# Optimization experiments

Measured on AMD Instinct MI355X. Metric: run time of the kernel, lower is better.

Reference implementation:

```python
import jax, jax.numpy as jnp
import numpy as np

T, TRACE, CTX = 4096, 64, 64


def setup_inputs() -> dict:
    key = jax.random.key(0)
    k0, k1, k2, k3 = jax.random.split(key, 4)
    state_re = jax.random.normal(k0, (T, TRACE, CTX), dtype=jnp.float32)
    state_im = jax.random.normal(k1, (T, TRACE, CTX), dtype=jnp.float32)
    x_re = jax.random.normal(k2, (T, TRACE, CTX), dtype=jnp.float32)
    x_im = jax.random.normal(k3, (T, TRACE, CTX), dtype=jnp.float32)
    # deterministic FFA param init (init_deterministic)
    a = jnp.linspace(1e-6, 0.5, TRACE).astype(jnp.float32)
    b = (2.0 * jnp.pi / jnp.linspace(1.0, 1000.0, CTX)).astype(jnp.float32)
    i = jnp.ones((T,), dtype=jnp.int32)          # carry step counter
    j = jnp.arange(T, dtype=jnp.int32)           # incoming time offsets
    return {"state_re": state_re, "state_im": state_im, "x_re": x_re,
            "x_im": x_im, "a": a, "b": b, "i": i, "j": j}


def reference(state_re, state_im, x_re, x_im, a, b, i, j):
    # gamma(t) = exp((-|a| + i*b) * t) expanded in real arithmetic
    t = j.astype(jnp.float32)[:, None, None]              # [T,1,1]
    decay = jnp.exp(-jnp.abs(a)[None, :, None] * t)       # [T,TRACE,1]
    theta = b[None, None, :] * t                          # [T,1,CTX]
    g_re = decay * jnp.cos(theta)                         # [T,TRACE,CTX]
    g_im = decay * jnp.sin(theta)
    # state * gamma + x  (complex multiply-add)
    new_re = state_re * g_re - state_im * g_im + x_re
    new_im = state_re * g_im + state_im * g_re + x_im
    # output: complex state stacked as (..., 2) = (re, im), plus updated counter
    return jnp.stack([new_re, new_im], axis=-1), j + i
```

## Files before the change

### kernel.cpp

```cpp
#include <hip/hip_runtime.h>
#include <math.h>

#define T_DIM 4096
#define TRACE 64
#define CTX 64

__global__ __launch_bounds__(256) void ffm_kernel(
    const float* __restrict__ state_re,
    const float* __restrict__ state_im,
    const float* __restrict__ x_re,
    const float* __restrict__ x_im,
    const float* __restrict__ a,
    const float* __restrict__ b,
    const int*   __restrict__ ivec,
    const int*   __restrict__ jvec,
    float* __restrict__ out,
    float* __restrict__ out_cnt)
{
    const int t   = blockIdx.x;
    const int tid = threadIdx.x;
    const float tf = (float)jvec[t];

    __shared__ float s_cos[CTX];
    __shared__ float s_sin[CTX];
    __shared__ float s_dec[TRACE];

    if (tid < CTX) {
        float theta = b[tid] * tf;
        float s, c;
        sincosf(theta, &s, &c);
        s_cos[tid] = c;
        s_sin[tid] = s;
    } else if (tid < CTX + TRACE) {
        int tr = tid - CTX;
        s_dec[tr] = expf(-fabsf(a[tr]) * tf);
    }
    if (tid == 0) {
        out_cnt[t] = (float)(jvec[t] + ivec[t]);
    }
    __syncthreads();

    const size_t base = (size_t)t * (TRACE * CTX);
    const float4* sre = (const float4*)(state_re + base);
    const float4* sim = (const float4*)(state_im + base);
    const float4* xre = (const float4*)(x_re + base);
    const float4* xim = (const float4*)(x_im + base);
    float4* o = (float4*)(out + base * 2);

    #pragma unroll
    for (int k = 0; k < 4; ++k) {
        const int g  = tid + k * 256;
        const int e  = g * 4;
        const int tr = e >> 6;
        const int c0 = e & 63;

        const float dec = s_dec[tr];
        const float4 vre = sre[g];
        const float4 vim = sim[g];
        const float4 vxr = xre[g];
        const float4 vxi = xim[g];

        const float gr0 = dec * s_cos[c0 + 0], gi0 = dec * s_sin[c0 + 0];
        const float gr1 = dec * s_cos[c0 + 1], gi1 = dec * s_sin[c0 + 1];
        const float gr2 = dec * s_cos[c0 + 2], gi2 = dec * s_sin[c0 + 2];
        const float gr3 = dec * s_cos[c0 + 3], gi3 = dec * s_sin[c0 + 3];

        float4 o0, o1;
        o0.x = fmaf(vre.x, gr0, fmaf(-vim.x, gi0, vxr.x));
        o0.y = fmaf(vre.x, gi0, fmaf( vim.x, gr0, vxi.x));
        o0.z = fmaf(vre.y, gr1, fmaf(-vim.y, gi1, vxr.y));
        o0.w = fmaf(vre.y, gi1, fmaf( vim.y, gr1, vxi.y));
        o1.x = fmaf(vre.z, gr2, fmaf(-vim.z, gi2, vxr.z));
        o1.y = fmaf(vre.z, gi2, fmaf( vim.z, gr2, vxi.z));
        o1.z = fmaf(vre.w, gr3, fmaf(-vim.w, gi3, vxr.w));
        o1.w = fmaf(vre.w, gi3, fmaf( vim.w, gr3, vxi.w));

        o[2 * g + 0] = o0;
        o[2 * g + 1] = o1;
    }
}

extern "C" void kernel_launch(void* const* d_in, const int* in_sizes, int n_in,
                              void* d_out, int out_size, void* d_ws, size_t ws_size,
                              hipStream_t stream) {
    const float* state_re = (const float*)d_in[0];
    const float* state_im = (const float*)d_in[1];
    const float* x_re     = (const float*)d_in[2];
    const float* x_im     = (const float*)d_in[3];
    const float* a        = (const float*)d_in[4];
    const float* b        = (const float*)d_in[5];
    const int*   iv       = (const int*)d_in[6];
    const int*   jv       = (const int*)d_in[7];

    float* out     = (float*)d_out;
    float* out_cnt = out + (size_t)T_DIM * TRACE * CTX * 2;

    ffm_kernel<<<T_DIM, 256, 0, stream>>>(state_re, state_im, x_re, x_im,
                                          a, b, iv, jv, out, out_cnt);
}
```

Measured before the change: 326.5 us.

## Precompute gamma tables in a separate kernel and stream main pass with grid-stride nontemporal stores

Moves the per-timestep sincos/exp computation into a small prepass kernel that writes cos, sin and decay tables to workspace. The main kernel then becomes a persistent grid-stride loop over 2048 blocks that reads the tables from global memory and writes the output with nontemporal stores. The aim is to remove per-block shared-memory setup and the __syncthreads barrier, and to keep streamed output from polluting the cache. In exchange it adds a second kernel launch and extra table traffic, and it falls back to the old kernel when the workspace is too small.

```diff
diff --git a/kernel.cpp b/kernel.cpp
--- a/kernel.cpp
+++ b/kernel.cpp
@@ -3,19 +3,89 @@
 
 #define T_DIM 4096
 #define TRACE 64
-#define CTX 64
+#define CTX   64
+#define NELEM  (T_DIM * TRACE * CTX)
+#define NGROUP (NELEM / 4)
 
-__global__ __launch_bounds__(256) void ffm_kernel(
-    const float* __restrict__ state_re,
-    const float* __restrict__ state_im,
-    const float* __restrict__ x_re,
-    const float* __restrict__ x_im,
-    const float* __restrict__ a,
-    const float* __restrict__ b,
-    const int*   __restrict__ ivec,
-    const int*   __restrict__ jvec,
-    float* __restrict__ out,
-    float* __restrict__ out_cnt)
+typedef float f32x4 __attribute__((ext_vector_type(4)));
+
+__global__ __launch_bounds__(256) void ffm_tables(
+    const float* __restrict__ a, const float* __restrict__ b,
+    const int*   __restrict__ iv, const int* __restrict__ jv,
+    float* __restrict__ tcos, float* __restrict__ tsin,
+    float* __restrict__ tdec, float* __restrict__ out_cnt)
+{
+    const int idx = blockIdx.x * 256 + threadIdx.x;
+    const int t   = idx >> 6;
+    const int k   = idx & 63;
+    const float tf = (float)jv[t];
+    float s, c;
+    sincosf(b[k] * tf, &s, &c);
+    tcos[idx] = c;
+    tsin[idx] = s;
+    tdec[idx] = expf(-fabsf(a[k]) * tf);
+    if (k == 0) out_cnt[t] = (float)(jv[t] + iv[t]);
+}
+
+__global__ __launch_bounds__(256) void ffm_main(
+    const float* __restrict__ sre_, const float* __restrict__ sim_,
+    const float* __restrict__ xre_, const float* __restrict__ xim_,
+    const float* __restrict__ tcos, const float* __restrict__ tsin,
+    const float* __restrict__ tdec,
+    float* __restrict__ out)
+{
+    const float4* __restrict__ sre = (const float4*)sre_;
+    const float4* __restrict__ sim = (const float4*)sim_;
+    const float4* __restrict__ xre = (const float4*)xre_;
+    const float4* __restrict__ xim = (const float4*)xim_;
+    f32x4* __restrict__ o = (f32x4*)out;
+
+    const int stride = gridDim.x * 256;
+    const int g0 = blockIdx.x * 256 + threadIdx.x;
+
+    #pragma unroll 2
+    for (int it = 0; it < NGROUP / (2048 * 256); ++it) {
+        const int g  = g0 + it * stride;
+        const int e  = g << 2;
+        const int t  = e >> 12;
+        const int tr = (e >> 6) & 63;
+        const int c0 = e & 63;
+
+        const float4 vc  = *(const float4*)(tcos + t * 64 + c0);
+        const float4 vs  = *(const float4*)(tsin + t * 64 + c0);
+        const float  dec = tdec[t * 64 + tr];
+
+        const float4 vre = sre[g];
+        const float4 vim = sim[g];
+        const float4 vxr = xre[g];
+        const float4 vxi = xim[g];
+
+        const float gr0 = dec * vc.x, gi0 = dec * vs.x;
+        const float gr1 = dec * vc.y, gi1 = dec * vs.y;
+        const float gr2 = dec * vc.z, gi2 = dec * vs.z;
+        const float gr3 = dec * vc.w, gi3 = dec * vs.w;
+
+        f32x4 o0, o1;
+        o0.x = fmaf(vre.x, gr0, fmaf(-vim.x, gi0, vxr.x));
+        o0.y = fmaf(vre.x, gi0, fmaf( vim.x, gr0, vxi.x));
+        o0.z = fmaf(vre.y, gr1, fmaf(-vim.y, gi1, vxr.y));
+        o0.w = fmaf(vre.y, gi1, fmaf( vim.y, gr1, vxi.y));
+        o1.x = fmaf(vre.z, gr2, fmaf(-vim.z, gi2, vxr.z));
+        o1.y = fmaf(vre.z, gi2, fmaf( vim.z, gr2, vxi.z));
+        o1.z = fmaf(vre.w, gr3, fmaf(-vim.w, gi3, vxr.w));
+        o1.w = fmaf(vre.w, gi3, fmaf( vim.w, gr3, vxi.w));
+
+        __builtin_nontemporal_store(o0, &o[2 * g + 0]);
+        __builtin_nontemporal_store(o1, &o[2 * g + 1]);
+    }
+}
+
+__global__ __launch_bounds__(256) void ffm_kernel_fallback(
+    const float* __restrict__ state_re, const float* __restrict__ state_im,
+    const float* __restrict__ x_re, const float* __restrict__ x_im,
+    const float* __restrict__ a, const float* __restrict__ b,
+    const int* __restrict__ ivec, const int* __restrict__ jvec,
+    float* __restrict__ out, float* __restrict__ out_cnt)
 {
     const int t   = blockIdx.x;
     const int tid = threadIdx.x;
@@ -35,9 +105,7 @@
         int tr = tid - CTX;
         s_dec[tr] = expf(-fabsf(a[tr]) * tf);
     }
-    if (tid == 0) {
-        out_cnt[t] = (float)(jvec[t] + ivec[t]);
-    }
+    if (tid == 0) out_cnt[t] = (float)(jvec[t] + ivec[t]);
     __syncthreads();
 
     const size_t base = (size_t)t * (TRACE * CTX);
@@ -95,6 +163,20 @@
     float* out     = (float*)d_out;
     float* out_cnt = out + (size_t)T_DIM * TRACE * CTX * 2;
 
-    ffm_kernel<<<T_DIM, 256, 0, stream>>>(state_re, state_im, x_re, x_im,
-                                          a, b, iv, jv, out, out_cnt);
+    const size_t tab_elems = (size_t)T_DIM * 64;
+    const size_t need = 3 * tab_elems * sizeof(float);
+
+    if (ws_size >= need) {
+        float* tcos = (float*)d_ws;
+        float* tsin = tcos + tab_elems;
+        float* tdec = tsin + tab_elems;
+
+        ffm_tables<<<T_DIM * 64 / 256, 256, 0, stream>>>(
+            a, b, iv, jv, tcos, tsin, tdec, out_cnt);
+        ffm_main<<<2048, 256, 0, stream>>>(
+            state_re, state_im, x_re, x_im, tcos, tsin, tdec, out);
+    } else {
+        ffm_kernel_fallback<<<T_DIM, 256, 0, stream>>>(
+            state_re, state_im, x_re, x_im, a, b, iv, jv, out, out_cnt);
+    }
 }
```

Measured after the change: 339.7 us. 4.1% more time.
